# Performance work log

Measured on AMD Instinct MI355X. Metric: run time of the kernel, lower is better.

The kernel has to match this reference:

```python
import jax, jax.numpy as jnp
import numpy as np

N, E, IN_F, H1, F1, H2, F2, OUT_F = 50000, 800000, 128, 4, 32, 1, 64, 2
NEG_SLOPE = 0.2  # PyG GATConv default


def setup_inputs() -> dict:
    key = jax.random.key(0)
    ks = jax.random.split(key, 10)
    p = lambda k, shp: jax.random.normal(k, shp, jnp.float32) * 0.1
    return {
        "x": jax.random.normal(ks[0], (N, IN_F), jnp.float32),
        "edge_index": jax.random.randint(ks[1], (2, E), 0, N),
        "W1": p(ks[2], (IN_F, H1 * F1)),
        "att_s1": p(ks[3], (H1, F1)),
        "att_d1": p(ks[4], (H1, F1)),
        "b1": jnp.zeros((H1 * F1,), jnp.float32),
        "W2": p(ks[5], (H1 * F1, H2 * F2)),
        "att_s2": p(ks[6], (H2, F2)),
        "att_d2": p(ks[7], (H2, F2)),
        "b2": jnp.zeros((F2,), jnp.float32),
        "Wl": p(ks[8], (F2, OUT_F)),
        "bl": jnp.zeros((OUT_F,), jnp.float32),
    }


def _gat_conv(x, src, dst, W, att_s, att_d, bias, concat):
    # PyG GATConv: per-head linear, leaky-relu attention logits,
    # segment-softmax over incoming edges of each dst, scatter-add aggregate.
    n = x.shape[0]
    H, F = att_s.shape
    h = (x @ W).reshape(n, H, F)                        # [N, H, F]
    a_s = jnp.einsum('nhf,hf->nh', h, att_s)            # [N, H]
    a_d = jnp.einsum('nhf,hf->nh', h, att_d)
    logits = jax.nn.leaky_relu(a_s[src] + a_d[dst], NEG_SLOPE)  # [Etot, H]
    m = jax.ops.segment_max(logits, dst, num_segments=n)
    e = jnp.exp(logits - m[dst])
    denom = jax.ops.segment_sum(e, dst, num_segments=n)
    alpha = e / denom[dst]                              # segment softmax
    msg = h[src] * alpha[:, :, None]                    # [Etot, H, F]
    out = jax.ops.segment_sum(msg, dst, num_segments=n)  # [N, H, F]
    out = out.reshape(n, H * F) if concat else out.mean(axis=1)
    return out + bias


def reference(x, edge_index, W1, att_s1, att_d1, b1, W2, att_s2, att_d2, b2, Wl, bl):
    n = x.shape[0]
    loops = jnp.arange(n, dtype=edge_index.dtype)       # add_self_loops=True
    src = jnp.concatenate([edge_index[0], loops])
    dst = jnp.concatenate([edge_index[1], loops])
    h = jax.nn.elu(_gat_conv(x, src, dst, W1, att_s1, att_d1, b1, True))
    h = jax.nn.elu(_gat_conv(h, src, dst, W2, att_s2, att_d2, b2, False))
    pooled = h.sum(axis=0, keepdims=True)               # global_add_pool, batch=0
    out = pooled @ Wl + bl
    return pooled, out
```

## Files before the change

### kernel.cpp

```cpp
#include <hip/hip_runtime.h>

#define N_NODES 50000
#define N_EDGES 800000
#define SCAN_BLOCKS ((N_NODES + 255) / 256)
#define HIST_BLOCKS ((N_EDGES + 255) / 256)
#define GEMM_BLOCKS ((N_NODES + 63) / 64)
#define FUSED_BLOCKS (5 * GEMM_BLOCKS)

__device__ __forceinline__ float lrelu(float x) { return fmaxf(x, 0.2f * x); }
__device__ __forceinline__ float elu(float x) { return x > 0.f ? x : __expf(x) - 1.f; }

typedef float f32x2 __attribute__((ext_vector_type(2)));

__device__ __forceinline__ float bfl(unsigned u) { return __uint_as_float(u << 16); }
__device__ __forceinline__ float bfh(unsigned u) { return __uint_as_float(u & 0xffff0000u); }
__device__ __forceinline__ unsigned f2bf_rn(float x) {
  unsigned u = __float_as_uint(x);
  return (u + 0x7fffu + ((u >> 16) & 1u)) >> 16;
}
__device__ __forceinline__ unsigned pack2bf(float a, float b) {
  return f2bf_rn(a) | (f2bf_rn(b) << 16);
}

__device__ __forceinline__ int block_excl_scan(int v, int* total_out) {
  int lane = threadIdx.x & 63;
  int wid = threadIdx.x >> 6;
  int x = v;
#pragma unroll
  for (int off = 1; off < 64; off <<= 1) {
    int u = __shfl_up(x, off);
    if (lane >= off) x += u;
  }
  __shared__ int wsum[4];
  if (lane == 63) wsum[wid] = x;
  __syncthreads();
  int add = 0;
#pragma unroll
  for (int k = 0; k < 4; ++k)
    if (k < wid) add += wsum[k];
  if (total_out) *total_out = wsum[0] + wsum[1] + wsum[2] + wsum[3];
  return x + add - v;
}

__global__ __launch_bounds__(256) void scan_part_kernel(const int* __restrict__ deg, int* __restrict__ rowptrP,
                                                        int* __restrict__ blocksum) {
  int g = blockIdx.x * 256 + threadIdx.x;
  int v = (g < N_NODES) ? deg[g] : 0;
  int total;
  int ex = block_excl_scan(v, &total);
  if (g < N_NODES) rowptrP[g] = ex;
  if (threadIdx.x == 0) blocksum[blockIdx.x] = total;
}

__global__ __launch_bounds__(256) void scan_top_kernel(const int* __restrict__ blocksum, int* __restrict__ blockoff) {
  int t = threadIdx.x;
  int v = (t < SCAN_BLOCKS) ? blocksum[t] : 0;
  int ex = block_excl_scan(v, nullptr);
  if (t < SCAN_BLOCKS) blockoff[t] = ex;
}

__global__ __launch_bounds__(256) void scatter_kernel(const int* __restrict__ ei, const int* __restrict__ rowptrP,
                                                      const int* __restrict__ blockoff, const int* __restrict__ rank,
                                                      int* __restrict__ col, int* __restrict__ rowptrF) {
  if (blockIdx.x < HIST_BLOCKS) {
    int e = blockIdx.x * 256 + threadIdx.x;
    if (e < N_EDGES) {
      int d = ei[N_EDGES + e];
      col[rowptrP[d] + blockoff[d >> 8] + rank[e]] = ei[e];
    }
  } else {
    int g = (blockIdx.x - HIST_BLOCKS) * 256 + threadIdx.x;
    if (g < N_NODES) rowptrF[g] = rowptrP[g] + blockoff[g >> 8];
    if (g == 0) rowptrF[N_NODES] = N_EDGES;
  }
}

#define XS_STRIDE 36
template <int COLS, bool ABF16>
__device__ __forceinline__ void gemm_body(int bx, const void* __restrict__ Ap, const float* __restrict__ W,
                                          const float* __restrict__ atts, const float* __restrict__ attd,
                                          unsigned* __restrict__ Yb, float* __restrict__ as_out,
                                          float* __restrict__ ad_out) {
  constexpr int CPT = COLS / 16;
  constexpr int G = COLS / 4;
  __shared__ float ws[32 * COLS];
  __shared__ float xs[64 * XS_STRIDE];
  int t = threadIdx.x;
  int rbase = bx * 64;
  int tx = t & 15, ty = t >> 4;
  float acc[4][CPT];
#pragma unroll
  for (int r = 0; r < 4; ++r)
#pragma unroll
    for (int c = 0; c < CPT; ++c) acc[r][c] = 0.f;

  const float4* W4 = (const float4*)W;
  float4* ws4 = (float4*)ws;
  for (int kt = 0; kt < 4; ++kt) {
    for (int i = t; i < 32 * G; i += 256) {
      int k = i / G;
      int g = i - k * G;
      int c4g = g & (CPT / 4 - 1);
      int txg = g / (CPT / 4);
      ws4[k * G + c4g * 16 + txg] = W4[kt * 32 * G + i];
    }
    if constexpr (ABF16) {
      const uint4* A4 = (const uint4*)Ap;
      {
        int i = t;
        int row = i >> 2, q = i & 3;
        int gr = rbase + row; if (gr >= N_NODES) gr = N_NODES - 1;
        uint4 u = A4[gr * 16 + kt * 4 + q];
        float4 lo = make_float4(bfl(u.x), bfh(u.x), bfl(u.y), bfh(u.y));
        float4 hi = make_float4(bfl(u.z), bfh(u.z), bfl(u.w), bfh(u.w));
        float4* dst = (float4*)&xs[row * XS_STRIDE + q * 8];
        dst[0] = lo; dst[1] = hi;
      }
    } else {
      const float4* A4 = (const float4*)Ap;
      for (int i = t; i < 512; i += 256) {
        int row = i >> 3, kc = i & 7;
        int gr = rbase + row; if (gr >= N_NODES) gr = N_NODES - 1;
        *(float4*)&xs[row * XS_STRIDE + kc * 4] = A4[gr * 32 + kt * 8 + kc];
      }
    }
    __syncthreads();
#pragma unroll 8
    for (int k = 0; k < 32; ++k) {
      float xr[4];
#pragma unroll
      for (int r = 0; r < 4; ++r) xr[r] = xs[(ty * 4 + r) * XS_STRIDE + k];
#pragma unroll
      for (int c4 = 0; c4 < CPT / 4; ++c4) {
        float4 wv = ws4[k * G + c4 * 16 + tx];
#pragma unroll
        for (int r = 0; r < 4; ++r) {
          acc[r][c4 * 4 + 0] += xr[r] * wv.x;
          acc[r][c4 * 4 + 1] += xr[r] * wv.y;
          acc[r][c4 * 4 + 2] += xr[r] * wv.z;
          acc[r][c4 * 4 + 3] += xr[r] * wv.w;
        }
      }
    }
    __syncthreads();
  }

  if constexpr (COLS == 128) {
    int h = tx >> 2;
    int base = h * 32 + (tx & 3) * 8;
#pragma unroll
    for (int r = 0; r < 4; ++r) {
      float ps = 0.f, pd = 0.f;
#pragma unroll
      for (int c = 0; c < 8; ++c) {
        ps += acc[r][c] * atts[base + c];
        pd += acc[r][c] * attd[base + c];
      }
      ps += __shfl_xor(ps, 1); pd += __shfl_xor(pd, 1);
      ps += __shfl_xor(ps, 2); pd += __shfl_xor(pd, 2);
      int row = rbase + ty * 4 + r;
      if ((tx & 3) == 0 && row < N_NODES) {
        as_out[row * 4 + h] = ps;
        ad_out[row * 4 + h] = pd;
      }
    }
  } else {
#pragma unroll
    for (int r = 0; r < 4; ++r) {
      float ps = 0.f, pd = 0.f;
#pragma unroll
      for (int c = 0; c < 4; ++c) {
        ps += acc[r][c] * atts[tx * 4 + c];
        pd += acc[r][c] * attd[tx * 4 + c];
      }
#pragma unroll
      for (int off = 1; off < 16; off <<= 1) {
        ps += __shfl_xor(ps, off);
        pd += __shfl_xor(pd, off);
      }
      int row = rbase + ty * 4 + r;
      if (tx == 0 && row < N_NODES) {
        as_out[row] = ps;
        ad_out[row] = pd;
      }
    }
  }

#pragma unroll
  for (int r = 0; r < 4; ++r) {
    int row = rbase + ty * 4 + r;
    if (row < N_NODES) {
      if constexpr (CPT == 8) {
        unsigned lo = __builtin_amdgcn_cvt_pk_fp8_f32(acc[r][0], acc[r][1], 0, false);
        lo = __builtin_amdgcn_cvt_pk_fp8_f32(acc[r][2], acc[r][3], lo, true);
        unsigned hi = __builtin_amdgcn_cvt_pk_fp8_f32(acc[r][4], acc[r][5], 0, false);
        hi = __builtin_amdgcn_cvt_pk_fp8_f32(acc[r][6], acc[r][7], hi, true);
        ((uint2*)Yb)[row * 16 + tx] = make_uint2(lo, hi);
      } else {
        unsigned u = __builtin_amdgcn_cvt_pk_fp8_f32(acc[r][0], acc[r][1], 0, false);
        u = __builtin_amdgcn_cvt_pk_fp8_f32(acc[r][2], acc[r][3], u, true);
        Yb[row * 16 + tx] = u;
      }
    }
  }
}

__global__ __launch_bounds__(256) void gemm128_hist_kernel(const float* __restrict__ x, const float* __restrict__ W1,
                                                           const float* __restrict__ atts, const float* __restrict__ attd,
                                                           unsigned* __restrict__ h1b, float* __restrict__ as1,
                                                           float* __restrict__ ad1, const int* __restrict__ ei,
                                                           int* __restrict__ deg, int* __restrict__ rank) {
  int role = blockIdx.x % 5;
  int base = blockIdx.x / 5;
  if (role != 4) {
    int e = (base * 4 + role) * 256 + threadIdx.x;
    if (e < N_EDGES) rank[e] = atomicAdd(&deg[ei[N_EDGES + e]], 1);
    return;
  }
  gemm_body<128, false>(base, x, W1, atts, attd, h1b, as1, ad1);
}

__global__ __launch_bounds__(256) void gemm64_kernel(const unsigned* __restrict__ h1eb, const float* __restrict__ W2,
                                                     const float* __restrict__ atts, const float* __restrict__ attd,
                                                     unsigned* __restrict__ h2b, float* __restrict__ as2,
                                                     float* __restrict__ ad2) {
  gemm_body<64, true>(blockIdx.x, h1eb, W2, atts, attd, h2b, as2, ad2);
}

__global__ __launch_bounds__(256) void agg1_kernel(const uint2* __restrict__ h1f8, const int* __restrict__ rowptr,
                                                   const int* __restrict__ col, const float* __restrict__ as1,
                                                   const float* __restrict__ ad1, const float4* __restrict__ b1v,
                                                   uint4* __restrict__ h1eb4) {
  int n = (blockIdx.x * 256 + threadIdx.x) >> 6;
  int lane = threadIdx.x & 63;
  int slot = lane >> 4;
  int fo = lane & 15;
  int h = fo >> 2;
  int beg = rowptr[n], end = rowptr[n + 1];
  float adh = ad1[n * 4 + h];

  f32x2 acc2[4];
#pragma unroll
  for (int j = 0; j < 4; ++j) acc2[j] = (f32x2){0.f, 0.f};
  float esum = 0.f;

#define ACC_EDGE1(E)                                               \
  {                                                                \
    int src = col[E];                                              \
    float a = __expf(lrelu(as1[src * 4 + h] + adh));               \
    esum += a;                                                     \
    f32x2 av = {a, a};                                             \
    uint2 uu = h1f8[src * 16 + fo];                                \
    f32x2 p0 = __builtin_amdgcn_cvt_pk_f32_fp8(uu.x, false);       \
    f32x2 p1 = __builtin_amdgcn_cvt_pk_f32_fp8(uu.x, true);        \
    f32x2 p2 = __builtin_amdgcn_cvt_pk_f32_fp8(uu.y, false);       \
    f32x2 p3 = __builtin_amdgcn_cvt_pk_f32_fp8(uu.y, true);        \
    acc2[0] += av * p0; acc2[1] += av * p1;                        \
    acc2[2] += av * p2; acc2[3] += av * p3;                        \
  }

  int i = beg;
  for (; i + 16 <= end; i += 16) {
#pragma unroll
    for (int u = 0; u < 4; ++u) ACC_EDGE1(i + u * 4 + slot);
  }
  for (; i + 4 <= end; i += 4) ACC_EDGE1(i + slot);
  int rem = end - i;
  if (slot < rem) ACC_EDGE1(i + slot);
#undef ACC_EDGE1
  if (slot == 0) {
    float a = __expf(lrelu(as1[n * 4 + h] + adh));
    esum += a;
    f32x2 av = {a, a};
    uint2 uu = h1f8[n * 16 + fo];
    f32x2 p0 = __builtin_amdgcn_cvt_pk_f32_fp8(uu.x, false);
    f32x2 p1 = __builtin_amdgcn_cvt_pk_f32_fp8(uu.x, true);
    f32x2 p2 = __builtin_amdgcn_cvt_pk_f32_fp8(uu.y, false);
    f32x2 p3 = __builtin_amdgcn_cvt_pk_f32_fp8(uu.y, true);
    acc2[0] += av * p0; acc2[1] += av * p1;
    acc2[2] += av * p2; acc2[3] += av * p3;
  }
#pragma unroll
  for (int j = 0; j < 4; ++j) {
    acc2[j].x += __shfl_xor(acc2[j].x, 16);
    acc2[j].y += __shfl_xor(acc2[j].y, 16);
    acc2[j].x += __shfl_xor(acc2[j].x, 32);
    acc2[j].y += __shfl_xor(acc2[j].y, 32);
  }
  esum += __shfl_xor(esum, 16);
  esum += __shfl_xor(esum, 32);
  if (slot == 0) {
    float dsc = 1.f / esum;
    float4 b0 = b1v[fo * 2], b1 = b1v[fo * 2 + 1];
    float f0 = elu(acc2[0].x * dsc + b0.x), f1 = elu(acc2[0].y * dsc + b0.y);
    float f2 = elu(acc2[1].x * dsc + b0.z), f3 = elu(acc2[1].y * dsc + b0.w);
    float f4 = elu(acc2[2].x * dsc + b1.x), f5 = elu(acc2[2].y * dsc + b1.y);
    float f6 = elu(acc2[3].x * dsc + b1.z), f7 = elu(acc2[3].y * dsc + b1.w);
    uint4 o;
    o.x = pack2bf(f0, f1); o.y = pack2bf(f2, f3);
    o.z = pack2bf(f4, f5); o.w = pack2bf(f6, f7);
    h1eb4[n * 16 + fo] = o;
  }
}

__global__ __launch_bounds__(256) void agg2_kernel(const uint2* __restrict__ h2f8, const int* __restrict__ rowptr,
                                                   const int* __restrict__ col, const float* __restrict__ as2,
                                                   const float* __restrict__ ad2, const float4* __restrict__ b2v,
                                                   float* __restrict__ pooled) {
  __shared__ float red[4][64];
  int n = (blockIdx.x * 256 + threadIdx.x) >> 6;
  int lane = threadIdx.x & 63;
  int wid = threadIdx.x >> 6;
  int slot = lane >> 3;
  int fo = lane & 7;
  int beg = rowptr[n], end = rowptr[n + 1];
  float ad = ad2[n];

  f32x2 acc2[4];
#pragma unroll
  for (int j = 0; j < 4; ++j) acc2[j] = (f32x2){0.f, 0.f};
  float esum = 0.f;

#define ACC_EDGE2(E)                                               \
  {                                                                \
    int src = col[E];                                              \
    float a = __expf(lrelu(as2[src] + ad));                        \
    esum += a;                                                     \
    f32x2 av = {a, a};                                             \
    uint2 uu = h2f8[src * 8 + fo];                                 \
    f32x2 p0 = __builtin_amdgcn_cvt_pk_f32_fp8(uu.x, false);       \
    f32x2 p1 = __builtin_amdgcn_cvt_pk_f32_fp8(uu.x, true);        \
    f32x2 p2 = __builtin_amdgcn_cvt_pk_f32_fp8(uu.y, false);       \
    f32x2 p3 = __builtin_amdgcn_cvt_pk_f32_fp8(uu.y, true);        \
    acc2[0] += av * p0; acc2[1] += av * p1;                        \
    acc2[2] += av * p2; acc2[3] += av * p3;                        \
  }

  int i = beg;
  for (; i + 32 <= end; i += 32) {
#pragma unroll
    for (int u = 0; u < 4; ++u) ACC_EDGE2(i + u * 8 + slot);
  }
  for (; i + 8 <= end; i += 8) ACC_EDGE2(i + slot);
  int rem = end - i;
  if (slot < rem) ACC_EDGE2(i + slot);
#undef ACC_EDGE2
  if (slot == 0) {
    float a = __expf(lrelu(as2[n] + ad));
    esum += a;
    f32x2 av = {a, a};
    uint2 uu = h2f8[n * 8 + fo];
    f32x2 p0 = __builtin_amdgcn_cvt_pk_f32_fp8(uu.x, false);
    f32x2 p1 = __builtin_amdgcn_cvt_pk_f32_fp8(uu.x, true);
    f32x2 p2 = __builtin_amdgcn_cvt_pk_f32_fp8(uu.y, false);
    f32x2 p3 = __builtin_amdgcn_cvt_pk_f32_fp8(uu.y, true);
    acc2[0] += av * p0; acc2[1] += av * p1;
    acc2[2] += av * p2; acc2[3] += av * p3;
  }
#pragma unroll
  for (int j = 0; j < 4; ++j) {
#pragma unroll
    for (int off = 8; off <= 32; off <<= 1) {
      acc2[j].x += __shfl_xor(acc2[j].x, off);
      acc2[j].y += __shfl_xor(acc2[j].y, off);
    }
  }
  esum += __shfl_xor(esum, 8);
  esum += __shfl_xor(esum, 16);
  esum += __shfl_xor(esum, 32);
  if (slot == 0) {
    float dsc = 1.f / esum;
    float4 b0 = b2v[fo * 2], b1 = b2v[fo * 2 + 1];
    red[wid][fo * 8 + 0] = elu(acc2[0].x * dsc + b0.x);
    red[wid][fo * 8 + 1] = elu(acc2[0].y * dsc + b0.y);
    red[wid][fo * 8 + 2] = elu(acc2[1].x * dsc + b0.z);
    red[wid][fo * 8 + 3] = elu(acc2[1].y * dsc + b0.w);
    red[wid][fo * 8 + 4] = elu(acc2[2].x * dsc + b1.x);
    red[wid][fo * 8 + 5] = elu(acc2[2].y * dsc + b1.y);
    red[wid][fo * 8 + 6] = elu(acc2[3].x * dsc + b1.z);
    red[wid][fo * 8 + 7] = elu(acc2[3].y * dsc + b1.w);
  }
  __syncthreads();
  if (threadIdx.x < 64) {
    float sum = red[0][threadIdx.x] + red[1][threadIdx.x] + red[2][threadIdx.x] + red[3][threadIdx.x];
    atomicAdd(&pooled[(blockIdx.x & 63) * 64 + threadIdx.x], sum);
  }
}

__global__ void final_kernel(const float* __restrict__ pooledS, const float* __restrict__ Wl,
                             const float* __restrict__ bl, float* __restrict__ out) {
  __shared__ float p[64];
  int t = threadIdx.x;
  float v = 0.f;
  for (int k = 0; k < 64; ++k) v += pooledS[k * 64 + t];
  p[t] = v;
  out[t] = v;
  __syncthreads();
  if (t < 2) {
    float s = bl[t];
    for (int k = 0; k < 64; ++k) s += p[k] * Wl[k * 2 + t];
    out[64 + t] = s;
  }
}

extern "C" void kernel_launch(void* const* d_in, const int* in_sizes, int n_in,
                              void* d_out, int out_size, void* d_ws, size_t ws_size,
                              hipStream_t stream) {
  (void)in_sizes; (void)n_in; (void)out_size; (void)ws_size;
  const float* x     = (const float*)d_in[0];
  const int*   ei    = (const int*)d_in[1];
  const float* W1    = (const float*)d_in[2];
  const float* atts1 = (const float*)d_in[3];
  const float* attd1 = (const float*)d_in[4];
  const float* b1    = (const float*)d_in[5];
  const float* W2    = (const float*)d_in[6];
  const float* atts2 = (const float*)d_in[7];
  const float* attd2 = (const float*)d_in[8];
  const float* b2    = (const float*)d_in[9];
  const float* Wl    = (const float*)d_in[10];
  const float* bl    = (const float*)d_in[11];
  float* out = (float*)d_out;

  char* w = (char*)d_ws;
  unsigned* h1b  = (unsigned*)w; w += (size_t)N_NODES * 128;
  unsigned* h1eb = (unsigned*)w; w += (size_t)N_NODES * 128 * 2;
  unsigned* h2b  = (unsigned*)w; w += (size_t)N_NODES * 64;
  float* as1  = (float*)w; w += (size_t)N_NODES * 16;
  float* ad1  = (float*)w; w += (size_t)N_NODES * 16;
  float* as2  = (float*)w; w += (size_t)N_NODES * 4;
  float* ad2  = (float*)w; w += (size_t)N_NODES * 4;
  int* deg    = (int*)w; w += (size_t)N_NODES * 4;
  float* pooled = (float*)w; w += 64 * 64 * 4;
  int* rowptrP = (int*)w; w += (size_t)(N_NODES + 1) * 4 + 12;
  int* rowptrF = (int*)w; w += (size_t)(N_NODES + 1) * 4 + 12;
  int* col    = (int*)w; w += (size_t)N_EDGES * 4;
  int* rank   = (int*)w; w += (size_t)N_EDGES * 4;
  int* blocksum = (int*)w; w += 256 * 4;
  int* blockoff = (int*)w; w += 256 * 4;

  (void)hipMemsetAsync(deg, 0, (size_t)N_NODES * 4 + 64 * 64 * 4, stream);

  gemm128_hist_kernel<<<FUSED_BLOCKS, 256, 0, stream>>>(x, W1, atts1, attd1, h1b, as1, ad1,
                                                        ei, deg, rank);
  scan_part_kernel<<<SCAN_BLOCKS, 256, 0, stream>>>(deg, rowptrP, blocksum);
  scan_top_kernel<<<1, 256, 0, stream>>>(blocksum, blockoff);
  scatter_kernel<<<HIST_BLOCKS + SCAN_BLOCKS, 256, 0, stream>>>(ei, rowptrP, blockoff, rank, col, rowptrF);

  agg1_kernel<<<N_NODES / 4, 256, 0, stream>>>((const uint2*)h1b, rowptrF, col, as1, ad1,
                                               (const float4*)b1, (uint4*)h1eb);

  gemm64_kernel<<<GEMM_BLOCKS, 256, 0, stream>>>(h1eb, W2, atts2, attd2, h2b, as2, ad2);
  agg2_kernel<<<N_NODES / 4, 256, 0, stream>>>((const uint2*)h2b, rowptrF, col, as2, ad2,
                                               (const float4*)b2, pooled);

  final_kernel<<<1, 64, 0, stream>>>(pooled, Wl, bl, out);
}
```

Baseline: 252.8 us.

## Replace global-atomic CSR build with two-pass bucketed counting sort

Replaces the per-edge global atomic degree count and rank-based scatter with a two-level radix-style sort. Dst values are first bucketed into 256-node bins using shared-memory histograms per edge chunk, then each bin is sorted locally in shared memory to produce the row pointers and column indices. The aim is to remove contended global atomics and random global scatters. In exchange it adds kernel launches and an intermediate edge buffer, and it un-fuses the histogram from the first GEMM, which now runs on its own.

```diff
diff --git a/kernel.cpp b/kernel.cpp
--- a/kernel.cpp
+++ b/kernel.cpp
@@ -2,10 +2,11 @@
 
 #define N_NODES 50000
 #define N_EDGES 800000
-#define SCAN_BLOCKS ((N_NODES + 255) / 256)
-#define HIST_BLOCKS ((N_EDGES + 255) / 256)
+#define NB 196
+#define P1_BLOCKS 256
+#define EPB 3125
+#define BH_SIZE (NB * P1_BLOCKS)
 #define GEMM_BLOCKS ((N_NODES + 63) / 64)
-#define FUSED_BLOCKS (5 * GEMM_BLOCKS)
 
 __device__ __forceinline__ float lrelu(float x) { return fmaxf(x, 0.2f * x); }
 __device__ __forceinline__ float elu(float x) { return x > 0.f ? x : __expf(x) - 1.f; }
@@ -42,36 +43,78 @@
   return x + add - v;
 }
 
-__global__ __launch_bounds__(256) void scan_part_kernel(const int* __restrict__ deg, int* __restrict__ rowptrP,
+__global__ __launch_bounds__(256) void hist1_kernel(const int* __restrict__ ei, int* __restrict__ bh) {
+  __shared__ int cnt[NB];
+  for (int t = threadIdx.x; t < NB; t += 256) cnt[t] = 0;
+  __syncthreads();
+  int start = blockIdx.x * EPB;
+  for (int i = start + threadIdx.x; i < start + EPB; i += 256)
+    atomicAdd(&cnt[ei[N_EDGES + i] >> 8], 1);
+  __syncthreads();
+  for (int t = threadIdx.x; t < NB; t += 256)
+    bh[t * P1_BLOCKS + blockIdx.x] = cnt[t];
+}
+
+__global__ __launch_bounds__(256) void scan_part_kernel(const int* __restrict__ bh, int* __restrict__ bhP,
                                                         int* __restrict__ blocksum) {
   int g = blockIdx.x * 256 + threadIdx.x;
-  int v = (g < N_NODES) ? deg[g] : 0;
+  int v = bh[g];
   int total;
   int ex = block_excl_scan(v, &total);
-  if (g < N_NODES) rowptrP[g] = ex;
+  bhP[g] = ex;
   if (threadIdx.x == 0) blocksum[blockIdx.x] = total;
 }
 
 __global__ __launch_bounds__(256) void scan_top_kernel(const int* __restrict__ blocksum, int* __restrict__ blockoff) {
   int t = threadIdx.x;
-  int v = (t < SCAN_BLOCKS) ? blocksum[t] : 0;
+  int v = (t < NB) ? blocksum[t] : 0;
   int ex = block_excl_scan(v, nullptr);
-  if (t < SCAN_BLOCKS) blockoff[t] = ex;
-}
-
-__global__ __launch_bounds__(256) void scatter_kernel(const int* __restrict__ ei, const int* __restrict__ rowptrP,
-                                                      const int* __restrict__ blockoff, const int* __restrict__ rank,
-                                                      int* __restrict__ col, int* __restrict__ rowptrF) {
-  if (blockIdx.x < HIST_BLOCKS) {
-    int e = blockIdx.x * 256 + threadIdx.x;
-    if (e < N_EDGES) {
-      int d = ei[N_EDGES + e];
-      col[rowptrP[d] + blockoff[d >> 8] + rank[e]] = ei[e];
-    }
-  } else {
-    int g = (blockIdx.x - HIST_BLOCKS) * 256 + threadIdx.x;
-    if (g < N_NODES) rowptrF[g] = rowptrP[g] + blockoff[g >> 8];
-    if (g == 0) rowptrF[N_NODES] = N_EDGES;
+  if (t < NB) blockoff[t] = ex;
+}
+
+__global__ __launch_bounds__(256) void scatter1_kernel(const int* __restrict__ ei, const int* __restrict__ bhP,
+                                                       const int* __restrict__ blockoff, int2* __restrict__ eb) {
+  __shared__ int cur[NB];
+  for (int t = threadIdx.x; t < NB; t += 256) cur[t] = 0;
+  __syncthreads();
+  int start = blockIdx.x * EPB;
+  for (int i = start + threadIdx.x; i < start + EPB; i += 256) {
+    int dst = ei[N_EDGES + i];
+    int src = ei[i];
+    int bin = dst >> 8;
+    int r = atomicAdd(&cur[bin], 1);
+    int idx = bin * P1_BLOCKS + blockIdx.x;
+    int pos = bhP[idx] + blockoff[bin] + r;
+    eb[pos] = make_int2(src, dst);
+  }
+}
+
+__global__ __launch_bounds__(256) void bucket_csr_kernel(const int2* __restrict__ eb, const int* __restrict__ blockoff,
+                                                         int* __restrict__ rowptrF, int* __restrict__ col) {
+  __shared__ int cnt[256];
+  __shared__ int basel[256];
+  __shared__ int cur[256];
+  int b = blockIdx.x;
+  int t = threadIdx.x;
+  cnt[t] = 0;
+  cur[t] = 0;
+  __syncthreads();
+  int start = blockoff[b];
+  int end = (b == NB - 1) ? N_EDGES : blockoff[b + 1];
+  for (int i = start + t; i < end; i += 256)
+    atomicAdd(&cnt[eb[i].y & 255], 1);
+  __syncthreads();
+  int ex = block_excl_scan(cnt[t], nullptr);
+  basel[t] = start + ex;
+  int g = b * 256 + t;
+  if (g < N_NODES) rowptrF[g] = start + ex;
+  if (g == N_NODES) rowptrF[N_NODES] = N_EDGES;
+  __syncthreads();
+  for (int i = start + t; i < end; i += 256) {
+    int2 e = eb[i];
+    int d8 = e.y & 255;
+    int r = atomicAdd(&cur[d8], 1);
+    col[basel[d8] + r] = e.x;
   }
 }
 
@@ -205,19 +248,11 @@
   }
 }
 
-__global__ __launch_bounds__(256) void gemm128_hist_kernel(const float* __restrict__ x, const float* __restrict__ W1,
-                                                           const float* __restrict__ atts, const float* __restrict__ attd,
-                                                           unsigned* __restrict__ h1b, float* __restrict__ as1,
-                                                           float* __restrict__ ad1, const int* __restrict__ ei,
-                                                           int* __restrict__ deg, int* __restrict__ rank) {
-  int role = blockIdx.x % 5;
-  int base = blockIdx.x / 5;
-  if (role != 4) {
-    int e = (base * 4 + role) * 256 + threadIdx.x;
-    if (e < N_EDGES) rank[e] = atomicAdd(&deg[ei[N_EDGES + e]], 1);
-    return;
-  }
-  gemm_body<128, false>(base, x, W1, atts, attd, h1b, as1, ad1);
+__global__ __launch_bounds__(256) void gemm128_kernel(const float* __restrict__ x, const float* __restrict__ W1,
+                                                      const float* __restrict__ atts, const float* __restrict__ attd,
+                                                      unsigned* __restrict__ h1b, float* __restrict__ as1,
+                                                      float* __restrict__ ad1) {
+  gemm_body<128, false>(blockIdx.x, x, W1, atts, attd, h1b, as1, ad1);
 }
 
 __global__ __launch_bounds__(256) void gemm64_kernel(const unsigned* __restrict__ h1eb, const float* __restrict__ W2,
@@ -429,23 +464,24 @@
   float* ad1  = (float*)w; w += (size_t)N_NODES * 16;
   float* as2  = (float*)w; w += (size_t)N_NODES * 4;
   float* ad2  = (float*)w; w += (size_t)N_NODES * 4;
-  int* deg    = (int*)w; w += (size_t)N_NODES * 4;
   float* pooled = (float*)w; w += 64 * 64 * 4;
-  int* rowptrP = (int*)w; w += (size_t)(N_NODES + 1) * 4 + 12;
   int* rowptrF = (int*)w; w += (size_t)(N_NODES + 1) * 4 + 12;
   int* col    = (int*)w; w += (size_t)N_EDGES * 4;
-  int* rank   = (int*)w; w += (size_t)N_EDGES * 4;
+  int2* eb    = (int2*)w; w += (size_t)N_EDGES * 8;
+  int* bh     = (int*)w; w += (size_t)BH_SIZE * 4;
+  int* bhP    = (int*)w; w += (size_t)BH_SIZE * 4;
   int* blocksum = (int*)w; w += 256 * 4;
   int* blockoff = (int*)w; w += 256 * 4;
 
-  (void)hipMemsetAsync(deg, 0, (size_t)N_NODES * 4 + 64 * 64 * 4, stream);
-
-  gemm128_hist_kernel<<<FUSED_BLOCKS, 256, 0, stream>>>(x, W1, atts1, attd1, h1b, as1, ad1,
-                                                        ei, deg, rank);
-  scan_part_kernel<<<SCAN_BLOCKS, 256, 0, stream>>>(deg, rowptrP, blocksum);
+  (void)hipMemsetAsync(pooled, 0, 64 * 64 * 4, stream);
+
+  hist1_kernel<<<P1_BLOCKS, 256, 0, stream>>>(ei, bh);
+  scan_part_kernel<<<BH_SIZE / 256, 256, 0, stream>>>(bh, bhP, blocksum);
   scan_top_kernel<<<1, 256, 0, stream>>>(blocksum, blockoff);
-  scatter_kernel<<<HIST_BLOCKS + SCAN_BLOCKS, 256, 0, stream>>>(ei, rowptrP, blockoff, rank, col, rowptrF);
-
+  scatter1_kernel<<<P1_BLOCKS, 256, 0, stream>>>(ei, bhP, blockoff, eb);
+  bucket_csr_kernel<<<NB, 256, 0, stream>>>(eb, blockoff, rowptrF, col);
+
+  gemm128_kernel<<<GEMM_BLOCKS, 256, 0, stream>>>(x, W1, atts1, attd1, h1b, as1, ad1);
   agg1_kernel<<<N_NODES / 4, 256, 0, stream>>>((const uint2*)h1b, rowptrF, col, as1, ad1,
                                                (const float4*)b1, (uint4*)h1eb);
 
```

Result: faster. 230.8 us (-8.7%).
